# Kernel tuning notes

Hardware: AMD Instinct MI355X
Metric: run time of the kernel (lower is better)

## Reference

```python
import jax, jax.numpy as jnp
import numpy as np

N = 10000       # nodes
E = 160000      # edges
D_IN = 256      # in_channels (node feature dim)
H1, C = 8, 32   # conv1: 8 heads x 32 -> 256; conv2: 1 head x 32
MSG = 128       # msg_dim
TD = 128        # time encoder out_channels
ED = MSG + TD   # edge_dim = 256
HC1 = H1 * C    # 256


def _lin(key, shape, scale=0.05):
    return jax.random.normal(key, shape, dtype=jnp.float32) * scale


def setup_inputs() -> dict:
    key = jax.random.key(0)
    ks = jax.random.split(key, 32)
    inp = {}
    inp["x"] = jax.random.normal(ks[0], (N, D_IN), dtype=jnp.float32)
    inp["last_update"] = jax.random.uniform(ks[1], (N,), jnp.float32, 0.0, 1000.0)
    inp["edge_index"] = jax.random.randint(ks[2], (2, E), 0, N)
    inp["t"] = jax.random.uniform(ks[3], (E,), jnp.float32, 0.0, 1000.0)
    inp["msg"] = jax.random.normal(ks[4], (E, MSG), dtype=jnp.float32)
    # TimeEncoder: Linear(1, TD) then cos
    inp["time_w"] = _lin(ks[5], (TD, 1), 0.1)
    inp["time_b"] = jnp.zeros((TD,), jnp.float32)
    # conv1 (TransformerConv in=256, heads=8, per-head 32, edge_dim=256, concat=True)
    inp["Wq1"] = _lin(ks[6], (D_IN, HC1)); inp["bq1"] = jnp.zeros((HC1,), jnp.float32)
    inp["Wk1"] = _lin(ks[7], (D_IN, HC1)); inp["bk1"] = jnp.zeros((HC1,), jnp.float32)
    inp["Wv1"] = _lin(ks[8], (D_IN, HC1)); inp["bv1"] = jnp.zeros((HC1,), jnp.float32)
    inp["We1"] = _lin(ks[9], (ED, HC1))   # lin_edge has no bias in PyG
    inp["Ws1"] = _lin(ks[10], (D_IN, HC1)); inp["bs1"] = jnp.zeros((HC1,), jnp.float32)
    # conv2 (in=256, heads=1, per-head 32, concat=False)
    inp["Wq2"] = _lin(ks[11], (HC1, C)); inp["bq2"] = jnp.zeros((C,), jnp.float32)
    inp["Wk2"] = _lin(ks[12], (HC1, C)); inp["bk2"] = jnp.zeros((C,), jnp.float32)
    inp["Wv2"] = _lin(ks[13], (HC1, C)); inp["bv2"] = jnp.zeros((C,), jnp.float32)
    inp["We2"] = _lin(ks[14], (ED, C))
    inp["Ws2"] = _lin(ks[15], (HC1, C)); inp["bs2"] = jnp.zeros((C,), jnp.float32)
    return inp


def transformer_conv(x, src, dst, edge_attr, Wq, bq, Wk, bk, Wv, bv, We, Ws, bs, heads, ch, concat):
    n = x.shape[0]
    q = (x @ Wq + bq).reshape(n, heads, ch)
    k = (x @ Wk + bk).reshape(n, heads, ch)
    v = (x @ Wv + bv).reshape(n, heads, ch)
    e = (edge_attr @ We).reshape(-1, heads, ch)       # [E,H,C]
    ke = k[src] + e                                    # key_j + edge
    ve = v[src] + e                                    # value_j + edge
    alpha = jnp.einsum('ehc,ehc->eh', q[dst], ke) / jnp.sqrt(jnp.float32(ch))
    # segment softmax over incoming edges of each destination node
    amax = jax.ops.segment_max(alpha, dst, num_segments=n)   # -inf for empty segs
    ex = jnp.exp(alpha - amax[dst])
    den = jax.ops.segment_sum(ex, dst, num_segments=n)
    attn = ex / (den[dst] + 1e-16)                     # [E,H]
    out = jax.ops.segment_sum(attn[:, :, None] * ve, dst, num_segments=n)  # [N,H,C]
    out = out.reshape(n, heads * ch) if concat else out.mean(axis=1)
    return out + (x @ Ws + bs)                         # root skip connection


def reference(x, last_update, edge_index, t, msg, time_w, time_b,
              Wq1, bq1, Wk1, bk1, Wv1, bv1, We1, Ws1, bs1,
              Wq2, bq2, Wk2, bk2, Wv2, bv2, We2, Ws2, bs2):
    src, dst = edge_index[0], edge_index[1]
    rel_t = last_update[src] - t                       # [E]
    rel_t_enc = jnp.cos(rel_t[:, None] * time_w[:, 0][None, :] + time_b)  # [E,TD]
    edge_attr = jnp.concatenate([rel_t_enc, msg], axis=-1)                # [E,ED]
    h = jax.nn.relu(transformer_conv(x, src, dst, edge_attr,
                                     Wq1, bq1, Wk1, bk1, Wv1, bv1, We1, Ws1, bs1,
                                     H1, C, True))
    out = jax.nn.relu(transformer_conv(h, src, dst, edge_attr,
                                       Wq2, bq2, Wk2, bk2, Wv2, bv2, We2, Ws2, bs2,
                                       1, C, False))
    return out
```

## Files before the change

kernel.cpp:

```cpp
#include <hip/hip_runtime.h>
#include <math.h>

#define N_NODES 10000
#define N_EDGES 160000
#define RT1 157
#define RTE 2500
#define CONVX_T (RT1 * 64 * 32)

static inline int ceildiv(int a, int b) { return (a + b - 1) / b; }

typedef float f32x4 __attribute__((ext_vector_type(4)));
typedef short bf16x8 __attribute__((ext_vector_type(8)));

__device__ __forceinline__ unsigned short f2bf(float f) {
  unsigned int u = __builtin_bit_cast(unsigned int, f);
  u += 0x7FFFu + ((u >> 16) & 1u);
  return (unsigned short)(u >> 16);
}
__device__ __forceinline__ float bf2f(unsigned short h) {
  unsigned int u = ((unsigned int)h) << 16;
  return __builtin_bit_cast(float, u);
}

__global__ void prep1_kernel(const float* __restrict__ lu, const int* __restrict__ srcp,
                             const int* __restrict__ dstp, const float* __restrict__ tt,
                             float* __restrict__ rel, int* __restrict__ deg, int E) {
  for (int i = blockIdx.x * blockDim.x + threadIdx.x; i < E; i += gridDim.x * blockDim.x) {
    rel[i] = lu[srcp[i]] - tt[i];
    atomicAdd(&deg[dstp[i]], 1);
  }
}

__global__ void scan_kernel(const int* __restrict__ deg, int* __restrict__ rowptr, int n) {
  __shared__ int part[1024];
  const int tid = threadIdx.x;
  const int CHK = 10;
  int base = tid * CHK;
  int loc[CHK];
  int s = 0;
#pragma unroll
  for (int j = 0; j < CHK; ++j) {
    int idx = base + j;
    int v = (idx < n) ? deg[idx] : 0;
    loc[j] = s; s += v;
  }
  part[tid] = s;
  __syncthreads();
  for (int off = 1; off < 1024; off <<= 1) {
    int y = (tid >= off) ? part[tid - off] : 0;
    __syncthreads();
    part[tid] += y;
    __syncthreads();
  }
  int pre = tid ? part[tid - 1] : 0;
#pragma unroll
  for (int j = 0; j < CHK; ++j) {
    int idx = base + j;
    if (idx < n) rowptr[idx] = pre + loc[j];
  }
  if (tid == 1023) rowptr[n] = part[1023];
}

__global__ void scatter_kernel(const int* __restrict__ srcp, const int* __restrict__ dstp,
                               const int* __restrict__ rowptr, int* __restrict__ fill,
                               int* __restrict__ sortpos, int* __restrict__ srcs, int E) {
  for (int e = blockIdx.x * blockDim.x + threadIdx.x; e < E; e += gridDim.x * blockDim.x) {
    int d = dstp[e];
    int pos = atomicAdd(&fill[d], 1);
    int slot = rowptr[d] + pos;
    sortpos[e] = slot;
    srcs[slot] = srcp[e];
  }
}

__device__ __forceinline__ void wstore(const float* __restrict__ W, unsigned short* __restrict__ out,
                                       int Nin, int n_off, int NFtot, int k, int c) {
  int gc = n_off + c;
  int ks=k>>5, kg=(k>>3)&3, j=k&7, nf=gc>>4, ic=gc&15;
  out[(size_t)(ks*NFtot+nf)*512 + (ic+16*kg)*8 + j] = f2bf(W[(size_t)k*Nin + c]);
}

__global__ void conv_all_kernel(const float* __restrict__ x, unsigned short* __restrict__ xa,
                                const float* Wq1, const float* Wk1, const float* Wv1, const float* Ws1,
                                const float* We1, const float* Wq2, const float* Wk2, const float* Wv2,
                                const float* Ws2, const float* We2,
                                const float* bq1, const float* bk1, const float* bv1, const float* bs1,
                                const float* bq2, const float* bk2, const float* bv2, const float* bs2,
                                unsigned short* W1f, unsigned short* We1f, unsigned short* W2f,
                                unsigned short* We2f, float* bcat1, float* bcat2) {
  int t0 = blockIdx.x * blockDim.x + threadIdx.x;
  if (t0 < CONVX_T) {
    int i = t0 >> 5, k8 = t0 & 31;
    union { uint4 q; unsigned short s[8]; } u;
    if (i < N_NODES) {
      const float4* px = (const float4*)(x + (size_t)i * 256 + k8 * 8);
      float4 f0 = px[0], f1 = px[1];
      u.s[0]=f2bf(f0.x); u.s[1]=f2bf(f0.y); u.s[2]=f2bf(f0.z); u.s[3]=f2bf(f0.w);
      u.s[4]=f2bf(f1.x); u.s[5]=f2bf(f1.y); u.s[6]=f2bf(f1.z); u.s[7]=f2bf(f1.w);
    } else {
      u.q = make_uint4(0,0,0,0);
    }
    int rt=i>>6, rf=(i>>4)&3, ir=i&15, ks=k8>>2, kg=k8&3;
    *(uint4*)&xa[(size_t)rt*16384 + ks*2048 + rf*512 + (ir+16*kg)*8] = u.q;
    return;
  }
  int t = t0 - CONVX_T;
  if (t < 262144) {
    int w = t >> 16, r = t & 65535, k = r >> 8, c = r & 255;
    const float* W = (w == 0) ? Wq1 : (w == 1) ? Wk1 : (w == 2) ? Wv1 : Ws1;
    wstore(W, W1f, 256, w * 256, 64, k, c);
  } else if (t < 327680) {
    int r = t - 262144, k = r >> 8, c = r & 255;
    wstore(We1, We1f, 256, 0, 16, k, c);
  } else if (t < 360448) {
    int r = t - 327680, w = r >> 13, r2 = r & 8191, k = r2 >> 5, c = r2 & 31;
    const float* W = (w == 0) ? Wq2 : (w == 1) ? Wk2 : (w == 2) ? Wv2 : Ws2;
    wstore(W, W2f, 32, w * 32, 8, k, c);
  } else if (t < 368640) {
    int r = t - 360448, k = r >> 5, c = r & 31;
    wstore(We2, We2f, 32, 0, 4, k, c);
  } else if (t < 369792) {
    int r = t - 368640;
    if (r < 1024) {
      const float* b = (r < 256) ? bq1 : (r < 512) ? bk1 : (r < 768) ? bv1 : bs1;
      bcat1[r] = b[r & 255];
    } else {
      int r2 = r - 1024;
      const float* b = (r2 < 32) ? bq2 : (r2 < 64) ? bk2 : (r2 < 96) ? bv2 : bs2;
      bcat2[r2] = b[r2 & 31];
    }
  }
}

__global__ __launch_bounds__(256)
void big_gemm(const unsigned short* __restrict__ xa, const unsigned short* __restrict__ W1f,
              const float* __restrict__ bcat1, float* __restrict__ qf,
              unsigned short* __restrict__ kvb, float* __restrict__ sf,
              const unsigned short* __restrict__ We1f, const unsigned short* __restrict__ We2f,
              unsigned short* __restrict__ e1b, unsigned short* __restrict__ e2b,
              const float* __restrict__ rel, const float* __restrict__ tw,
              const float* __restrict__ tb, const float* __restrict__ msg,
              const int* __restrict__ sortpos) {
  __shared__ char ldsraw[38912];
  uint4* lds4 = (uint4*)ldsraw;
  const int tid = threadIdx.x;
  const int wid = tid >> 6, lane = tid & 63;
  const int bx = blockIdx.x;

  if (bx < RTE) {
    const int rt0 = bx;
    const int phase = bx & 7;
    const int arf = tid >> 6, ar2 = tid & 63, air = ar2 & 15, akg = ar2 >> 4;
    const int aedge = rt0 * 64 + arf * 16 + air;

    {
      float rl = rel[aedge];
#pragma unroll
      for (int s = 0; s < 4; ++s) {
        int k8 = s * 4 + akg;
        const float4* twp = (const float4*)(tw + k8 * 8);
        const float4* tbp = (const float4*)(tb + k8 * 8);
        float4 w0 = twp[0], w1 = twp[1], b0 = tbp[0], b1 = tbp[1];
        union { uint4 q; unsigned short us[8]; } u;
        u.us[0]=f2bf(__cosf(rl*w0.x+b0.x)); u.us[1]=f2bf(__cosf(rl*w0.y+b0.y));
        u.us[2]=f2bf(__cosf(rl*w0.z+b0.z)); u.us[3]=f2bf(__cosf(rl*w0.w+b0.w));
        u.us[4]=f2bf(__cosf(rl*w1.x+b1.x)); u.us[5]=f2bf(__cosf(rl*w1.y+b1.y));
        u.us[6]=f2bf(__cosf(rl*w1.z+b1.z)); u.us[7]=f2bf(__cosf(rl*w1.w+b1.w));
        lds4[s * 256 + tid] = u.q;
      }
    }

    auto fetchMsg = [&](int ks) -> uint4 {
      const float4* pm = (const float4*)(msg + (size_t)aedge * 128 + (size_t)(ks * 4 + akg - 16) * 8);
      float4 f0 = pm[0], f1 = pm[1];
      union { uint4 q; unsigned short us[8]; } u;
      u.us[0]=f2bf(f0.x); u.us[1]=f2bf(f0.y); u.us[2]=f2bf(f0.z); u.us[3]=f2bf(f0.w);
      u.us[4]=f2bf(f1.x); u.us[5]=f2bf(f1.y); u.us[6]=f2bf(f1.z); u.us[7]=f2bf(f1.w);
      return u.q;
    };
    auto fetchB = [&](int ks, int p) -> uint4 {
      return *(const uint4*)(We1f + (size_t)ks * 8192 + (size_t)(tid + p * 256) * 8);
    };
    auto fetchB2 = [&](int ks) -> uint4 {
      return *(const uint4*)(We2f + (size_t)(ks * 4 + (tid >> 6)) * 512 + (size_t)(tid & 63) * 8);
    };

    uint4 rB[2][4];
    uint4 rA[2];
    uint4 rB2 = make_uint4(0, 0, 0, 0);
    {
      int ks0 = 0 ^ phase, ks1 = 1 ^ phase;
#pragma unroll
      for (int p = 0; p < 4; ++p) rB[0][p] = fetchB(ks0, p);
#pragma unroll
      for (int p = 0; p < 4; ++p) rB[1][p] = fetchB(ks1, p);
      if (ks0 >= 4) rA[0] = fetchMsg(ks0);
      if (ks1 >= 4) rA[1] = fetchMsg(ks1);
      if (tid < 128) rB2 = fetchB2(ks0);
    }

    f32x4 acc[4][4];
    f32x4 acc2[4];
#pragma unroll
    for (int i = 0; i < 4; ++i) {
      acc2[i] = (f32x4){0.f, 0.f, 0.f, 0.f};
#pragma unroll
      for (int j = 0; j < 4; ++j) acc[i][j] = (f32x4){0.f, 0.f, 0.f, 0.f};
    }

#pragma unroll
    for (int ksi = 0; ksi < 8; ++ksi) {
      const int ks = ksi ^ phase;
      const int sl = ksi & 1;
      __syncthreads();
#pragma unroll
      for (int p = 0; p < 4; ++p) lds4[1280 + tid + p * 256] = rB[sl][p];
      if (tid < 128) lds4[2304 + tid] = rB2;
      if (ks >= 4) lds4[1024 + tid] = rA[sl];
      if (ksi < 6) {
        int kf = (ksi + 2) ^ phase;
#pragma unroll
        for (int p = 0; p < 4; ++p) rB[sl][p] = fetchB(kf, p);
        if (kf >= 4) rA[sl] = fetchMsg(kf);
      }
      if (ksi < 7) {
        int kf1 = (ksi + 1) ^ phase;
        if (tid < 128) rB2 = fetchB2(kf1);
      }
      __syncthreads();
      bf16x8 a[4], b[4];
      const uint4* abase = (ks < 4) ? &lds4[ks * 256] : &lds4[1024];
#pragma unroll
      for (int rf = 0; rf < 4; ++rf) a[rf] = *(const bf16x8*)&abase[rf * 64 + lane];
#pragma unroll
      for (int cf = 0; cf < 4; ++cf) b[cf] = *(const bf16x8*)&lds4[1280 + (wid * 4 + cf) * 64 + lane];
#pragma unroll
      for (int rf = 0; rf < 4; ++rf)
#pragma unroll
        for (int cf = 0; cf < 4; ++cf)
          acc[rf][cf] = __builtin_amdgcn_mfma_f32_16x16x32_bf16(a[rf], b[cf], acc[rf][cf], 0, 0, 0);
      if (wid < 2) {
        bf16x8 b2 = *(const bf16x8*)&lds4[2304 + wid * 64 + lane];
#pragma unroll
        for (int rf = 0; rf < 4; ++rf)
          acc2[rf] = __builtin_amdgcn_mfma_f32_16x16x32_bf16(a[rf], b2, acc2[rf], 0, 0, 0);
      }
    }

    __syncthreads();
    unsigned short* cl  = (unsigned short*)ldsraw;
    unsigned short* cl2 = (unsigned short*)(ldsraw + 9216);
    int* spos = (int*)(ldsraw + 14336);
    if (tid < 64) spos[tid] = sortpos[rt0 * 64 + tid];
    const int fr0 = (lane >> 4) * 4;
    const int fc0 = lane & 15;
    if (wid < 2) {
#pragma unroll
      for (int rf = 0; rf < 4; ++rf)
#pragma unroll
        for (int j = 0; j < 4; ++j)
          cl2[(fr0 + rf * 16 + j) * 40 + wid * 16 + fc0] = f2bf(acc2[rf][j]);
    }
    for (int pass = 0; pass < 4; ++pass) {
      if (wid == pass) {
#pragma unroll
        for (int cf = 0; cf < 4; ++cf) {
          int c = fc0 + cf * 16;
#pragma unroll
          for (int rf = 0; rf < 4; ++rf)
#pragma unroll
            for (int j = 0; j < 4; ++j)
              cl[(fr0 + rf * 16 + j) * 72 + c] = f2bf(acc[rf][cf][j]);
        }
      }
      __syncthreads();
#pragma unroll
      for (int id = tid; id < 512; id += 256) {
        int row = id >> 3, cc = (id & 7) * 8;
        int gr = spos[row];
        *(uint4*)&e1b[(size_t)gr * 256 + pass * 64 + cc] = *(const uint4*)&cl[row * 72 + cc];
      }
      __syncthreads();
    }
    {
      int row = tid >> 2, cc = (tid & 3) * 8;
      int gr = spos[row];
      *(uint4*)&e2b[(size_t)gr * 32 + cc] = *(const uint4*)&cl2[row * 40 + cc];
    }
  } else {
    const int idx = bx - RTE;
    const int rt0 = idx % RT1;
    const int y = idx / RT1;
    const int phase = rt0 & 7;
    const int n0f = y * 16;

    auto fetchA = [&](int ks) -> uint4 {
      return *(const uint4*)(xa + (size_t)rt0 * 16384 + (size_t)ks * 2048 + (size_t)tid * 8);
    };
    auto fetchB = [&](int ks, int p) -> uint4 {
      return *(const uint4*)(W1f + ((size_t)ks * 64 + n0f) * 512 + (size_t)(tid + p * 256) * 8);
    };

    uint4 stA0 = fetchA(0 ^ phase);
    uint4 stA1 = fetchA(1 ^ phase);
    uint4 stB[4];
#pragma unroll
    for (int p = 0; p < 4; ++p) stB[p] = fetchB(0 ^ phase, p);

    f32x4 acc[4][4];
#pragma unroll
    for (int i = 0; i < 4; ++i)
#pragma unroll
      for (int j = 0; j < 4; ++j) acc[i][j] = (f32x4){0.f, 0.f, 0.f, 0.f};

#pragma unroll
    for (int ksi = 0; ksi < 8; ++ksi) {
      __syncthreads();
      lds4[tid] = ((ksi & 1) == 0) ? stA0 : stA1;
#pragma unroll
      for (int p = 0; p < 4; ++p) lds4[256 + tid + p * 256] = stB[p];
      if (ksi < 6) {
        int kf = (ksi + 2) ^ phase;
        if ((ksi & 1) == 0) stA0 = fetchA(kf); else stA1 = fetchA(kf);
      }
      if (ksi < 7) {
        int kf1 = (ksi + 1) ^ phase;
#pragma unroll
        for (int p = 0; p < 4; ++p) stB[p] = fetchB(kf1, p);
      }
      __syncthreads();
      bf16x8 a[4], b[4];
#pragma unroll
      for (int rf = 0; rf < 4; ++rf) a[rf] = *(const bf16x8*)&lds4[rf * 64 + lane];
#pragma unroll
      for (int cf = 0; cf < 4; ++cf) b[cf] = *(const bf16x8*)&lds4[256 + (wid * 4 + cf) * 64 + lane];
#pragma unroll
      for (int rf = 0; rf < 4; ++rf)
#pragma unroll
        for (int cf = 0; cf < 4; ++cf)
          acc[rf][cf] = __builtin_amdgcn_mfma_f32_16x16x32_bf16(a[rf], b[cf], acc[rf][cf], 0, 0, 0);
    }

    bool bf16path;
    void* dstp_; int cstr_, dc0_, bcol0_;
    if (y == 0)      { bf16path = false; dstp_ = qf;  cstr_ = 256; dc0_ = 0;   bcol0_ = 0; }
    else if (y == 1) { bf16path = true;  dstp_ = kvb; cstr_ = 512; dc0_ = 0;   bcol0_ = 256; }
    else if (y == 2) { bf16path = true;  dstp_ = kvb; cstr_ = 512; dc0_ = 256; bcol0_ = 512; }
    else             { bf16path = false; dstp_ = sf;  cstr_ = 256; dc0_ = 0;   bcol0_ = 768; }
    const int fr0 = (lane >> 4) * 4;
    const int fc0 = lane & 15;
    if (!bf16path) {
      float* dst = (float*)dstp_;
      const int row0 = rt0 * 64 + fr0;
      const int cb2 = wid * 64 + fc0;
#pragma unroll
      for (int cf = 0; cf < 4; ++cf) {
        int c = cb2 + cf * 16;
        float bv = bcat1[bcol0_ + c];
#pragma unroll
        for (int rf = 0; rf < 4; ++rf) {
#pragma unroll
          for (int j = 0; j < 4; ++j) {
            int r = row0 + rf * 16 + j;
            if (r < N_NODES) dst[(size_t)r * cstr_ + c] = acc[rf][cf][j] + bv;
          }
        }
      }
    } else {
      __syncthreads();
      unsigned short* cl = (unsigned short*)ldsraw;
      unsigned short* dst = (unsigned short*)dstp_;
      for (int pass = 0; pass < 4; ++pass) {
        if (wid == pass) {
#pragma unroll
          for (int cf = 0; cf < 4; ++cf) {
            int c = fc0 + cf * 16;
            float bv = bcat1[bcol0_ + pass * 64 + c];
#pragma unroll
            for (int rf = 0; rf < 4; ++rf)
#pragma unroll
              for (int j = 0; j < 4; ++j)
                cl[(fr0 + rf * 16 + j) * 72 + c] = f2bf(acc[rf][cf][j] + bv);
          }
        }
        __syncthreads();
#pragma unroll
        for (int id = tid; id < 512; id += 256) {
          int row = id >> 3, cc = (id & 7) * 8;
          int gr = rt0 * 64 + row;
          if (gr < N_NODES)
            *(uint4*)&dst[(size_t)gr * cstr_ + dc0_ + pass * 64 + cc] = *(const uint4*)&cl[row * 72 + cc];
        }
        __syncthreads();
      }
    }
  }
}

__global__ __launch_bounds__(256)
void gemm_node2(const unsigned short* __restrict__ ha, const unsigned short* __restrict__ W2f,
                const float* __restrict__ bcat2, float* __restrict__ qkvs2) {
  __shared__ uint4 lds4[1024];
  const int tid = threadIdx.x;
  const int wid = tid >> 6, lane = tid & 63;
  const int wr = wid >> 1, wc = wid & 1;
  const int rt0 = blockIdx.x * 2;
  const int phase = blockIdx.x & 7;

  auto fetchA = [&](int ks, int p) -> uint4 {
    int c = tid + p * 256;
    int rt = rt0 + (c >> 8);
    if (rt >= RT1) rt = RT1 - 1;
    return *(const uint4*)(ha + (size_t)rt * 16384 + (size_t)ks * 2048 + (size_t)(c & 255) * 8);
  };
  auto fetchB = [&](int ks, int p) -> uint4 {
    return *(const uint4*)(W2f + (size_t)ks * 8 * 512 + (size_t)(tid + p * 256) * 8);
  };

  uint4 stA0[2], stA1[2], stB[2];
#pragma unroll
  for (int p = 0; p < 2; ++p) stA0[p] = fetchA(0 ^ phase, p);
#pragma unroll
  for (int p = 0; p < 2; ++p) stA1[p] = fetchA(1 ^ phase, p);
#pragma unroll
  for (int p = 0; p < 2; ++p) stB[p] = fetchB(0 ^ phase, p);

  f32x4 acc[4][4];
#pragma unroll
  for (int i = 0; i < 4; ++i)
#pragma unroll
    for (int j = 0; j < 4; ++j) acc[i][j] = (f32x4){0.f, 0.f, 0.f, 0.f};

#pragma unroll
  for (int ksi = 0; ksi < 8; ++ksi) {
    __syncthreads();
#pragma unroll
    for (int p = 0; p < 2; ++p) lds4[tid + p * 256] = ((ksi & 1) == 0) ? stA0[p] : stA1[p];
#pragma unroll
    for (int p = 0; p < 2; ++p) lds4[512 + tid + p * 256] = stB[p];
    if (ksi < 6) {
      int kf = (ksi + 2) ^ phase;
      if ((ksi & 1) == 0) {
#pragma unroll
        for (int p = 0; p < 2; ++p) stA0[p] = fetchA(kf, p);
      } else {
#pragma unroll
        for (int p = 0; p < 2; ++p) stA1[p] = fetchA(kf, p);
      }
    }
    if (ksi < 7) {
      int kf1 = (ksi + 1) ^ phase;
#pragma unroll
      for (int p = 0; p < 2; ++p) stB[p] = fetchB(kf1, p);
    }
    __syncthreads();
    bf16x8 a[4], b[4];
#pragma unroll
    for (int rf = 0; rf < 4; ++rf) a[rf] = *(const bf16x8*)&lds4[(wr * 4 + rf) * 64 + lane];
#pragma unroll
    for (int cf = 0; cf < 4; ++cf) b[cf] = *(const bf16x8*)&lds4[512 + (wc * 4 + cf) * 64 + lane];
#pragma unroll
    for (int rf = 0; rf < 4; ++rf)
#pragma unroll
      for (int cf = 0; cf < 4; ++cf)
        acc[rf][cf] = __builtin_amdgcn_mfma_f32_16x16x32_bf16(a[rf], b[cf], acc[rf][cf], 0, 0, 0);
  }

  const int row0 = (rt0 + wr) * 64 + ((lane >> 4) * 4);
  const int cb2 = wc * 64 + (lane & 15);
#pragma unroll
  for (int cf = 0; cf < 4; ++cf) {
    int c = cb2 + cf * 16;
    float bv = bcat2[c];
#pragma unroll
    for (int rf = 0; rf < 4; ++rf) {
#pragma unroll
      for (int j = 0; j < 4; ++j) {
        int r = row0 + rf * 16 + j;
        if (r < N_NODES) qkvs2[(size_t)r * 128 + c] = acc[rf][cf][j] + bv;
      }
    }
  }
}

__global__ __launch_bounds__(64)
void attn1_kernel(const float* __restrict__ qf, const unsigned short* __restrict__ kvb,
                  const float* __restrict__ sf, const unsigned short* __restrict__ e1b,
                  const int* __restrict__ srcs, const int* __restrict__ rowptr,
                  unsigned short* __restrict__ ha) {
  const int n = blockIdx.x;
  const int lane = threadIdx.x;
  const int h = lane >> 3;
  const int c0 = (lane & 7) * 4;
  const int off = h * 32 + c0;
  const int beg = rowptr[n], end = rowptr[n + 1];
  const float4 q = *(const float4*)&qf[(size_t)n * 256 + off];
  float m0 = -INFINITY, d0 = 0.f, x0 = 0.f, x1 = 0.f, x2 = 0.f, x3 = 0.f;
  float m1 = -INFINITY, d1 = 0.f, y0 = 0.f, y1 = 0.f, y2 = 0.f, y3 = 0.f;
  int i = beg;
  for (; i + 1 < end; i += 2) {
    const int sA = srcs[i], sB = srcs[i + 1];
    ushort4 evA = *(const ushort4*)&e1b[(size_t)i * 256 + off];
    ushort4 kkA = *(const ushort4*)&kvb[(size_t)sA * 512 + off];
    ushort4 vvA = *(const ushort4*)&kvb[(size_t)sA * 512 + 256 + off];
    ushort4 evB = *(const ushort4*)&e1b[(size_t)(i + 1) * 256 + off];
    ushort4 kkB = *(const ushort4*)&kvb[(size_t)sB * 512 + off];
    ushort4 vvB = *(const ushort4*)&kvb[(size_t)sB * 512 + 256 + off];
    float eA0=bf2f(evA.x), eA1=bf2f(evA.y), eA2=bf2f(evA.z), eA3=bf2f(evA.w);
    float eB0=bf2f(evB.x), eB1=bf2f(evB.y), eB2=bf2f(evB.z), eB3=bf2f(evB.w);
    float pA = q.x*(bf2f(kkA.x)+eA0) + q.y*(bf2f(kkA.y)+eA1) + q.z*(bf2f(kkA.z)+eA2) + q.w*(bf2f(kkA.w)+eA3);
    float pB = q.x*(bf2f(kkB.x)+eB0) + q.y*(bf2f(kkB.y)+eB1) + q.z*(bf2f(kkB.z)+eB2) + q.w*(bf2f(kkB.w)+eB3);
    pA += __shfl_xor(pA, 1); pA += __shfl_xor(pA, 2); pA += __shfl_xor(pA, 4);
    pB += __shfl_xor(pB, 1); pB += __shfl_xor(pB, 2); pB += __shfl_xor(pB, 4);
    pA *= 0.17677669529663687f;
    pB *= 0.17677669529663687f;
    {
      const float mn = fmaxf(m0, pA);
      const float sc = __expf(m0 - mn), w = __expf(pA - mn);
      d0 = d0 * sc + w;
      x0 = x0 * sc + w * (bf2f(vvA.x) + eA0);
      x1 = x1 * sc + w * (bf2f(vvA.y) + eA1);
      x2 = x2 * sc + w * (bf2f(vvA.z) + eA2);
      x3 = x3 * sc + w * (bf2f(vvA.w) + eA3);
      m0 = mn;
    }
    {
      const float mn = fmaxf(m1, pB);
      const float sc = __expf(m1 - mn), w = __expf(pB - mn);
      d1 = d1 * sc + w;
      y0 = y0 * sc + w * (bf2f(vvB.x) + eB0);
      y1 = y1 * sc + w * (bf2f(vvB.y) + eB1);
      y2 = y2 * sc + w * (bf2f(vvB.z) + eB2);
      y3 = y3 * sc + w * (bf2f(vvB.w) + eB3);
      m1 = mn;
    }
  }
  if (i < end) {
    const int sA = srcs[i];
    ushort4 evA = *(const ushort4*)&e1b[(size_t)i * 256 + off];
    ushort4 kkA = *(const ushort4*)&kvb[(size_t)sA * 512 + off];
    ushort4 vvA = *(const ushort4*)&kvb[(size_t)sA * 512 + 256 + off];
    float eA0=bf2f(evA.x), eA1=bf2f(evA.y), eA2=bf2f(evA.z), eA3=bf2f(evA.w);
    float pA = q.x*(bf2f(kkA.x)+eA0) + q.y*(bf2f(kkA.y)+eA1) + q.z*(bf2f(kkA.z)+eA2) + q.w*(bf2f(kkA.w)+eA3);
    pA += __shfl_xor(pA, 1); pA += __shfl_xor(pA, 2); pA += __shfl_xor(pA, 4);
    pA *= 0.17677669529663687f;
    const float mn = fmaxf(m0, pA);
    const float sc = __expf(m0 - mn), w = __expf(pA - mn);
    d0 = d0 * sc + w;
    x0 = x0 * sc + w * (bf2f(vvA.x) + eA0);
    x1 = x1 * sc + w * (bf2f(vvA.y) + eA1);
    x2 = x2 * sc + w * (bf2f(vvA.z) + eA2);
    x3 = x3 * sc + w * (bf2f(vvA.w) + eA3);
    m0 = mn;
  }
  float den = d0, a0 = x0, a1 = x1, a2 = x2, a3 = x3;
  if (m1 != -INFINITY) {
    const float M = fmaxf(m0, m1);
    const float sA = __expf(m0 - M), sB = __expf(m1 - M);
    den = d0 * sA + d1 * sB;
    a0 = x0 * sA + y0 * sB; a1 = x1 * sA + y1 * sB;
    a2 = x2 * sA + y2 * sB; a3 = x3 * sA + y3 * sB;
  }
  const float inv = 1.f / (den + 1e-16f);
  const float4 sk = *(const float4*)&sf[(size_t)n * 256 + off];
  float o0 = fmaxf(a0 * inv + sk.x, 0.f);
  float o1 = fmaxf(a1 * inv + sk.y, 0.f);
  float o2 = fmaxf(a2 * inv + sk.z, 0.f);
  float o3 = fmaxf(a3 * inv + sk.w, 0.f);
  int rt = n >> 6, rf = (n >> 4) & 3, ir = n & 15;
  int kg = (lane & 7) >> 1, jj = 4 * (lane & 1);
  ushort4 w4;
  w4.x = f2bf(o0); w4.y = f2bf(o1); w4.z = f2bf(o2); w4.w = f2bf(o3);
  *(ushort4*)&ha[(size_t)rt * 16384 + h * 2048 + rf * 512 + (ir + 16 * kg) * 8 + jj] = w4;
}

__global__ __launch_bounds__(64)
void attn2_kernel(const float* __restrict__ qkvs2, const unsigned short* __restrict__ e2b,
                  const int* __restrict__ srcs, const int* __restrict__ rowptr,
                  float* __restrict__ outp) {
  const int n = blockIdx.x;
  const int tid = threadIdx.x;
  const int c = tid & 31;
  const int beg = rowptr[n], end = rowptr[n + 1];
  const float qv = qkvs2[(size_t)n * 128 + c];
  float m0 = -INFINITY, d0 = 0.f, x0 = 0.f;
  float m1 = -INFINITY, d1 = 0.f, y0 = 0.f;
  int i = beg;
  for (; i + 1 < end; i += 2) {
    const int sA = srcs[i], sB = srcs[i + 1];
    const float eA = bf2f(e2b[(size_t)i * 32 + c]);
    const float eB = bf2f(e2b[(size_t)(i + 1) * 32 + c]);
    float pA = qv * (qkvs2[(size_t)sA * 128 + 32 + c] + eA);
    float pB = qv * (qkvs2[(size_t)sB * 128 + 32 + c] + eB);
    const float vA = qkvs2[(size_t)sA * 128 + 64 + c] + eA;
    const float vB = qkvs2[(size_t)sB * 128 + 64 + c] + eB;
#pragma unroll
    for (int off = 16; off; off >>= 1) pA += __shfl_xor(pA, off);
#pragma unroll
    for (int off = 16; off; off >>= 1) pB += __shfl_xor(pB, off);
    pA *= 0.17677669529663687f;
    pB *= 0.17677669529663687f;
    {
      const float mn = fmaxf(m0, pA);
      const float sc = __expf(m0 - mn), w = __expf(pA - mn);
      d0 = d0 * sc + w; x0 = x0 * sc + w * vA; m0 = mn;
    }
    {
      const float mn = fmaxf(m1, pB);
      const float sc = __expf(m1 - mn), w = __expf(pB - mn);
      d1 = d1 * sc + w; y0 = y0 * sc + w * vB; m1 = mn;
    }
  }
  if (i < end) {
    const int sA = srcs[i];
    const float eA = bf2f(e2b[(size_t)i * 32 + c]);
    float pA = qv * (qkvs2[(size_t)sA * 128 + 32 + c] + eA);
    const float vA = qkvs2[(size_t)sA * 128 + 64 + c] + eA;
#pragma unroll
    for (int off = 16; off; off >>= 1) pA += __shfl_xor(pA, off);
    pA *= 0.17677669529663687f;
    const float mn = fmaxf(m0, pA);
    const float sc = __expf(m0 - mn), w = __expf(pA - mn);
    d0 = d0 * sc + w; x0 = x0 * sc + w * vA; m0 = mn;
  }
  float den = d0, acc = x0;
  if (m1 != -INFINITY) {
    const float M = fmaxf(m0, m1);
    const float sA = __expf(m0 - M), sB = __expf(m1 - M);
    den = d0 * sA + d1 * sB;
    acc = x0 * sA + y0 * sB;
  }
  if (tid < 32) {
    float o = acc / (den + 1e-16f) + qkvs2[(size_t)n * 128 + 96 + c];
    outp[(size_t)n * 32 + c] = fmaxf(o, 0.f);
  }
}

extern "C" void kernel_launch(void* const* d_in, const int* in_sizes, int n_in,
                              void* d_out, int out_size, void* d_ws, size_t ws_size,
                              hipStream_t stream) {
  const float* x   = (const float*)d_in[0];
  const float* lu  = (const float*)d_in[1];
  const int*   ei  = (const int*)d_in[2];
  const float* tt  = (const float*)d_in[3];
  const float* msg = (const float*)d_in[4];
  const float* tw  = (const float*)d_in[5];
  const float* tb  = (const float*)d_in[6];
  const float* Wq1 = (const float*)d_in[7];  const float* bq1 = (const float*)d_in[8];
  const float* Wk1 = (const float*)d_in[9];  const float* bk1 = (const float*)d_in[10];
  const float* Wv1 = (const float*)d_in[11]; const float* bv1 = (const float*)d_in[12];
  const float* We1 = (const float*)d_in[13];
  const float* Ws1 = (const float*)d_in[14]; const float* bs1 = (const float*)d_in[15];
  const float* Wq2 = (const float*)d_in[16]; const float* bq2 = (const float*)d_in[17];
  const float* Wk2 = (const float*)d_in[18]; const float* bk2 = (const float*)d_in[19];
  const float* Wv2 = (const float*)d_in[20]; const float* bv2 = (const float*)d_in[21];
  const float* We2 = (const float*)d_in[22];
  const float* Ws2 = (const float*)d_in[23]; const float* bs2 = (const float*)d_in[24];

  const int* srcp = ei;
  const int* dstp = ei + N_EDGES;

  char* p = (char*)d_ws;
  auto alloc = [&](size_t bytes) -> char* {
    char* r = p;
    p += (bytes + 255) & ~(size_t)255;
    return r;
  };
  int*   deg     = (int*)alloc((size_t)N_NODES * 4);
  int*   fill    = (int*)alloc((size_t)N_NODES * 4);
  int*   rowptr  = (int*)alloc((size_t)(N_NODES + 1) * 4);
  int*   sortpos = (int*)alloc((size_t)N_EDGES * 4);
  int*   srcs    = (int*)alloc((size_t)N_EDGES * 4);
  float* rel     = (float*)alloc((size_t)N_EDGES * 4);
  unsigned short* xa   = (unsigned short*)alloc((size_t)RT1 * 32768);
  unsigned short* W1f  = (unsigned short*)alloc((size_t)8 * 64 * 1024);
  unsigned short* We1f = (unsigned short*)alloc((size_t)8 * 16 * 1024);
  unsigned short* W2f  = (unsigned short*)alloc((size_t)8 * 8 * 1024);
  unsigned short* We2f = (unsigned short*)alloc((size_t)8 * 4 * 1024);
  float* bcat1  = (float*)alloc(1024 * 4);
  float* bcat2  = (float*)alloc(128 * 4);
  float* qf     = (float*)alloc((size_t)N_NODES * 256 * 4);
  unsigned short* kvb = (unsigned short*)alloc((size_t)N_NODES * 512 * 2);
  float* sf     = (float*)alloc((size_t)N_NODES * 256 * 4);
  unsigned short* e1b = (unsigned short*)alloc((size_t)N_EDGES * 256 * 2);
  unsigned short* ha  = (unsigned short*)alloc((size_t)RT1 * 32768);
  float* qkvs2  = (float*)alloc((size_t)N_NODES * 128 * 4);
  unsigned short* e2b = (unsigned short*)alloc((size_t)N_EDGES * 32 * 2);
  float* outp   = (float*)d_out;

  hipMemsetAsync(deg, 0, (size_t)N_NODES * 4, stream);
  hipMemsetAsync(fill, 0, (size_t)N_NODES * 4, stream);
  hipMemsetAsync(ha + (size_t)(RT1 - 1) * 16384, 0, 32768, stream);

  prep1_kernel<<<625, 256, 0, stream>>>(lu, srcp, dstp, tt, rel, deg, N_EDGES);
  scan_kernel<<<1, 1024, 0, stream>>>(deg, rowptr, N_NODES);
  scatter_kernel<<<625, 256, 0, stream>>>(srcp, dstp, rowptr, fill, sortpos, srcs, N_EDGES);

  conv_all_kernel<<<ceildiv(CONVX_T + 369792, 256), 256, 0, stream>>>(
      x, xa, Wq1, Wk1, Wv1, Ws1, We1, Wq2, Wk2, Wv2, Ws2, We2,
      bq1, bk1, bv1, bs1, bq2, bk2, bv2, bs2,
      W1f, We1f, W2f, We2f, bcat1, bcat2);

  big_gemm<<<RTE + RT1 * 4, 256, 0, stream>>>(
      xa, W1f, bcat1, qf, kvb, sf, We1f, We2f, e1b, e2b,
      rel, tw, tb, msg, sortpos);

  attn1_kernel<<<N_NODES, 64, 0, stream>>>(qf, kvb, sf, e1b, srcs, rowptr, ha);
  gemm_node2<<<ceildiv(RT1, 2), 256, 0, stream>>>(ha, W2f, bcat2, qkvs2);
  attn2_kernel<<<N_NODES, 64, 0, stream>>>(qkvs2, e2b, srcs, rowptr, outp);
}
```

Before: 191.9 us.

## Read GEMM B operands directly from global and stage the full A tile in LDS once

All three GEMM paths (edge GEMM, node GEMM and gemm_node2) drop the register-staged, double-buffered LDS pipeline. The full A tile (time encoding plus msg, or xa) is now written to LDS once before the loop, and the B fragments (weights) are loaded per wave straight from global memory, which should hit in cache. This removes two barriers per k-step and the LDS store traffic for B. The cost is that global weight-load latency is exposed inside the MFMA loop with no prefetch. gemm_node2 also reads its A fragments directly from global.

```diff
diff --git a/kernel.cpp b/kernel.cpp
--- a/kernel.cpp
+++ b/kernel.cpp
@@ -141,7 +141,7 @@
               const float* __restrict__ rel, const float* __restrict__ tw,
               const float* __restrict__ tb, const float* __restrict__ msg,
               const int* __restrict__ sortpos) {
-  __shared__ char ldsraw[38912];
+  __shared__ char ldsraw[32768];
   uint4* lds4 = (uint4*)ldsraw;
   const int tid = threadIdx.x;
   const int wid = tid >> 6, lane = tid & 63;
@@ -168,36 +168,17 @@
         u.us[6]=f2bf(__cosf(rl*w1.z+b1.z)); u.us[7]=f2bf(__cosf(rl*w1.w+b1.w));
         lds4[s * 256 + tid] = u.q;
       }
-    }
-
-    auto fetchMsg = [&](int ks) -> uint4 {
-      const float4* pm = (const float4*)(msg + (size_t)aedge * 128 + (size_t)(ks * 4 + akg - 16) * 8);
-      float4 f0 = pm[0], f1 = pm[1];
-      union { uint4 q; unsigned short us[8]; } u;
-      u.us[0]=f2bf(f0.x); u.us[1]=f2bf(f0.y); u.us[2]=f2bf(f0.z); u.us[3]=f2bf(f0.w);
-      u.us[4]=f2bf(f1.x); u.us[5]=f2bf(f1.y); u.us[6]=f2bf(f1.z); u.us[7]=f2bf(f1.w);
-      return u.q;
-    };
-    auto fetchB = [&](int ks, int p) -> uint4 {
-      return *(const uint4*)(We1f + (size_t)ks * 8192 + (size_t)(tid + p * 256) * 8);
-    };
-    auto fetchB2 = [&](int ks) -> uint4 {
-      return *(const uint4*)(We2f + (size_t)(ks * 4 + (tid >> 6)) * 512 + (size_t)(tid & 63) * 8);
-    };
-
-    uint4 rB[2][4];
-    uint4 rA[2];
-    uint4 rB2 = make_uint4(0, 0, 0, 0);
-    {
-      int ks0 = 0 ^ phase, ks1 = 1 ^ phase;
-#pragma unroll
-      for (int p = 0; p < 4; ++p) rB[0][p] = fetchB(ks0, p);
-#pragma unroll
-      for (int p = 0; p < 4; ++p) rB[1][p] = fetchB(ks1, p);
-      if (ks0 >= 4) rA[0] = fetchMsg(ks0);
-      if (ks1 >= 4) rA[1] = fetchMsg(ks1);
-      if (tid < 128) rB2 = fetchB2(ks0);
-    }
+#pragma unroll
+      for (int s = 0; s < 4; ++s) {
+        const float4* pm = (const float4*)(msg + (size_t)aedge * 128 + (size_t)(s * 4 + akg) * 8);
+        float4 f0 = pm[0], f1 = pm[1];
+        union { uint4 q; unsigned short us[8]; } u;
+        u.us[0]=f2bf(f0.x); u.us[1]=f2bf(f0.y); u.us[2]=f2bf(f0.z); u.us[3]=f2bf(f0.w);
+        u.us[4]=f2bf(f1.x); u.us[5]=f2bf(f1.y); u.us[6]=f2bf(f1.z); u.us[7]=f2bf(f1.w);
+        lds4[(4 + s) * 256 + tid] = u.q;
+      }
+    }
+    __syncthreads();
 
     f32x4 acc[4][4];
     f32x4 acc2[4];
@@ -211,36 +192,20 @@
 #pragma unroll
     for (int ksi = 0; ksi < 8; ++ksi) {
       const int ks = ksi ^ phase;
-      const int sl = ksi & 1;
-      __syncthreads();
-#pragma unroll
-      for (int p = 0; p < 4; ++p) lds4[1280 + tid + p * 256] = rB[sl][p];
-      if (tid < 128) lds4[2304 + tid] = rB2;
-      if (ks >= 4) lds4[1024 + tid] = rA[sl];
-      if (ksi < 6) {
-        int kf = (ksi + 2) ^ phase;
-#pragma unroll
-        for (int p = 0; p < 4; ++p) rB[sl][p] = fetchB(kf, p);
-        if (kf >= 4) rA[sl] = fetchMsg(kf);
-      }
-      if (ksi < 7) {
-        int kf1 = (ksi + 1) ^ phase;
-        if (tid < 128) rB2 = fetchB2(kf1);
-      }
-      __syncthreads();
       bf16x8 a[4], b[4];
-      const uint4* abase = (ks < 4) ? &lds4[ks * 256] : &lds4[1024];
+      const uint4* abase = &lds4[ks * 256];
 #pragma unroll
       for (int rf = 0; rf < 4; ++rf) a[rf] = *(const bf16x8*)&abase[rf * 64 + lane];
 #pragma unroll
-      for (int cf = 0; cf < 4; ++cf) b[cf] = *(const bf16x8*)&lds4[1280 + (wid * 4 + cf) * 64 + lane];
+      for (int cf = 0; cf < 4; ++cf)
+        b[cf] = *(const bf16x8*)(We1f + ((size_t)(ks * 16 + wid * 4 + cf)) * 512 + (size_t)lane * 8);
+      bf16x8 b2 = *(const bf16x8*)(We2f + ((size_t)(ks * 4 + (wid & 1))) * 512 + (size_t)lane * 8);
 #pragma unroll
       for (int rf = 0; rf < 4; ++rf)
 #pragma unroll
         for (int cf = 0; cf < 4; ++cf)
           acc[rf][cf] = __builtin_amdgcn_mfma_f32_16x16x32_bf16(a[rf], b[cf], acc[rf][cf], 0, 0, 0);
       if (wid < 2) {
-        bf16x8 b2 = *(const bf16x8*)&lds4[2304 + wid * 64 + lane];
 #pragma unroll
         for (int rf = 0; rf < 4; ++rf)
           acc2[rf] = __builtin_amdgcn_mfma_f32_16x16x32_bf16(a[rf], b2, acc2[rf], 0, 0, 0);
@@ -294,18 +259,10 @@
     const int phase = rt0 & 7;
     const int n0f = y * 16;
 
-    auto fetchA = [&](int ks) -> uint4 {
-      return *(const uint4*)(xa + (size_t)rt0 * 16384 + (size_t)ks * 2048 + (size_t)tid * 8);
-    };
-    auto fetchB = [&](int ks, int p) -> uint4 {
-      return *(const uint4*)(W1f + ((size_t)ks * 64 + n0f) * 512 + (size_t)(tid + p * 256) * 8);
-    };
-
-    uint4 stA0 = fetchA(0 ^ phase);
-    uint4 stA1 = fetchA(1 ^ phase);
-    uint4 stB[4];
-#pragma unroll
-    for (int p = 0; p < 4; ++p) stB[p] = fetchB(0 ^ phase, p);
+#pragma unroll
+    for (int s = 0; s < 8; ++s)
+      lds4[s * 256 + tid] = *(const uint4*)(xa + (size_t)rt0 * 16384 + (size_t)s * 2048 + (size_t)tid * 8);
+    __syncthreads();
 
     f32x4 acc[4][4];
 #pragma unroll
@@ -315,25 +272,13 @@
 
 #pragma unroll
     for (int ksi = 0; ksi < 8; ++ksi) {
-      __syncthreads();
-      lds4[tid] = ((ksi & 1) == 0) ? stA0 : stA1;
-#pragma unroll
-      for (int p = 0; p < 4; ++p) lds4[256 + tid + p * 256] = stB[p];
-      if (ksi < 6) {
-        int kf = (ksi + 2) ^ phase;
-        if ((ksi & 1) == 0) stA0 = fetchA(kf); else stA1 = fetchA(kf);
-      }
-      if (ksi < 7) {
-        int kf1 = (ksi + 1) ^ phase;
-#pragma unroll
-        for (int p = 0; p < 4; ++p) stB[p] = fetchB(kf1, p);
-      }
-      __syncthreads();
+      const int ks = ksi ^ phase;
       bf16x8 a[4], b[4];
 #pragma unroll
-      for (int rf = 0; rf < 4; ++rf) a[rf] = *(const bf16x8*)&lds4[rf * 64 + lane];
-#pragma unroll
-      for (int cf = 0; cf < 4; ++cf) b[cf] = *(const bf16x8*)&lds4[256 + (wid * 4 + cf) * 64 + lane];
+      for (int rf = 0; rf < 4; ++rf) a[rf] = *(const bf16x8*)&lds4[ks * 256 + rf * 64 + lane];
+#pragma unroll
+      for (int cf = 0; cf < 4; ++cf)
+        b[cf] = *(const bf16x8*)(W1f + ((size_t)(ks * 64 + n0f + wid * 4 + cf)) * 512 + (size_t)lane * 8);
 #pragma unroll
       for (int rf = 0; rf < 4; ++rf)
 #pragma unroll
@@ -400,30 +345,12 @@
 __global__ __launch_bounds__(256)
 void gemm_node2(const unsigned short* __restrict__ ha, const unsigned short* __restrict__ W2f,
                 const float* __restrict__ bcat2, float* __restrict__ qkvs2) {
-  __shared__ uint4 lds4[1024];
   const int tid = threadIdx.x;
   const int wid = tid >> 6, lane = tid & 63;
   const int wr = wid >> 1, wc = wid & 1;
   const int rt0 = blockIdx.x * 2;
-  const int phase = blockIdx.x & 7;
-
-  auto fetchA = [&](int ks, int p) -> uint4 {
-    int c = tid + p * 256;
-    int rt = rt0 + (c >> 8);
-    if (rt >= RT1) rt = RT1 - 1;
-    return *(const uint4*)(ha + (size_t)rt * 16384 + (size_t)ks * 2048 + (size_t)(c & 255) * 8);
-  };
-  auto fetchB = [&](int ks, int p) -> uint4 {
-    return *(const uint4*)(W2f + (size_t)ks * 8 * 512 + (size_t)(tid + p * 256) * 8);
-  };
-
-  uint4 stA0[2], stA1[2], stB[2];
-#pragma unroll
-  for (int p = 0; p < 2; ++p) stA0[p] = fetchA(0 ^ phase, p);
-#pragma unroll
-  for (int p = 0; p < 2; ++p) stA1[p] = fetchA(1 ^ phase, p);
-#pragma unroll
-  for (int p = 0; p < 2; ++p) stB[p] = fetchB(0 ^ phase, p);
+  int rtA = rt0 + wr;
+  if (rtA >= RT1) rtA = RT1 - 1;
 
   f32x4 acc[4][4];
 #pragma unroll
@@ -432,33 +359,14 @@
     for (int j = 0; j < 4; ++j) acc[i][j] = (f32x4){0.f, 0.f, 0.f, 0.f};
 
 #pragma unroll
-  for (int ksi = 0; ksi < 8; ++ksi) {
-    __syncthreads();
-#pragma unroll
-    for (int p = 0; p < 2; ++p) lds4[tid + p * 256] = ((ksi & 1) == 0) ? stA0[p] : stA1[p];
-#pragma unroll
-    for (int p = 0; p < 2; ++p) lds4[512 + tid + p * 256] = stB[p];
-    if (ksi < 6) {
-      int kf = (ksi + 2) ^ phase;
-      if ((ksi & 1) == 0) {
-#pragma unroll
-        for (int p = 0; p < 2; ++p) stA0[p] = fetchA(kf, p);
-      } else {
-#pragma unroll
-        for (int p = 0; p < 2; ++p) stA1[p] = fetchA(kf, p);
-      }
-    }
-    if (ksi < 7) {
-      int kf1 = (ksi + 1) ^ phase;
-#pragma unroll
-      for (int p = 0; p < 2; ++p) stB[p] = fetchB(kf1, p);
-    }
-    __syncthreads();
+  for (int ks = 0; ks < 8; ++ks) {
     bf16x8 a[4], b[4];
 #pragma unroll
-    for (int rf = 0; rf < 4; ++rf) a[rf] = *(const bf16x8*)&lds4[(wr * 4 + rf) * 64 + lane];
-#pragma unroll
-    for (int cf = 0; cf < 4; ++cf) b[cf] = *(const bf16x8*)&lds4[512 + (wc * 4 + cf) * 64 + lane];
+    for (int rf = 0; rf < 4; ++rf)
+      a[rf] = *(const bf16x8*)(ha + (size_t)rtA * 16384 + (size_t)ks * 2048 + (size_t)(rf * 64 + lane) * 8);
+#pragma unroll
+    for (int cf = 0; cf < 4; ++cf)
+      b[cf] = *(const bf16x8*)(W2f + ((size_t)(ks * 8 + wc * 4 + cf)) * 512 + (size_t)lane * 8);
 #pragma unroll
     for (int rf = 0; rf < 4; ++rf)
 #pragma unroll
```

Result: slower. 199.3 us (+3.8%).
